# Performance work log

Measured on AMD Instinct MI355X. Metric: run time of the kernel, lower is better.

## Reference

```python
import jax, jax.numpy as jnp
import numpy as np

K = 2          # hops
N_HEAD = 34    # relation types
H = 100        # hidden size
BS = 32
N_NODE = 200
EPS = 1e-20
INIT_RANGE = 0.01


def setup_inputs() -> dict:
    key = jax.random.key(0)
    ks = jax.random.split(key, 7)
    X = jax.random.normal(ks[0], (BS, N_NODE, H), dtype=jnp.float32)
    A = (jax.random.uniform(ks[1], (BS, N_HEAD, N_NODE, N_NODE)) < 0.05).astype(jnp.float32)
    start_attn = jax.random.uniform(ks[2], (BS, N_NODE), dtype=jnp.float32)
    end_attn = jax.random.uniform(ks[3], (BS, N_NODE), dtype=jnp.float32)
    uni_attn = jax.random.uniform(ks[4], (BS, N_HEAD), dtype=jnp.float32)
    trans_attn = jax.random.uniform(ks[5], (BS, N_HEAD, N_HEAD), dtype=jnp.float32)
    # dense branch: diag_decompose=False, n_basis=0 -> (k, n_head+1, h, h)
    w_vs = jax.random.uniform(ks[6], (K, N_HEAD + 1, H, H), dtype=jnp.float32,
                              minval=-INIT_RANGE, maxval=INIT_RANGE)
    return dict(X=X, A=A, start_attn=start_attn, end_attn=end_attn,
                uni_attn=uni_attn, trans_attn=trans_attn, w_vs=w_vs)


def reference(X, A, start_attn, end_attn, uni_attn, trans_attn, w_vs):
    # _get_weights (n_basis == 0, diag_decompose == False)
    W = w_vs[:, :-1]   # (k, n_head, h, h)
    Wi = w_vs[:, -1]   # (k, h, h)
    W_pad = [jnp.eye(H, dtype=X.dtype)]
    for t in range(K - 1):
        W_pad = [Wi[K - 1 - t] @ W_pad[0]] + W_pad   # length k

    # ---- Z propagation ----
    Z0 = X * start_attn[:, :, None]                  # (b, n, h)
    Z_all = []
    Zprev = None                                     # (b, f, n, h) after a hop
    for t in range(K):
        if t == 0:
            Zin = jnp.broadcast_to(Z0[:, :, :, None], (BS, N_NODE, H, N_HEAD))
        else:
            # permute + bmm with trans_attn: mix over incoming head f -> g
            Zin = jnp.einsum('bfni,bfg->bnig', Zprev, trans_attn)
        # per-head feature transform: (b,n,i,f) x (f,i,o) -> (b,f,n,o)
        Zh = jnp.einsum('bnif,fio->bfno', Zin, W[t])
        Zh = Zh * uni_attn[:, :, None, None]
        # adjacency propagation per head: A (b,f,m,n) x Z (b,f,n,o)
        Zh = jnp.einsum('bfmn,bfno->bfmo', A, Zh)    # (b, f, n, h)
        # sum heads, project with W_pad[t], gate by end_attn
        Zt = jnp.einsum('bfno,oi->bni', Zh, W_pad[t])
        Zt = Zt * end_attn[:, :, None]
        Z_all.append(Zt)
        Zprev = Zh

    # ---- degree normalizer D ----
    D_all = []
    Dprev = None                                     # (b, f, n)
    for t in range(K):
        if t == 0:
            Din = jnp.broadcast_to(start_attn[:, None, :], (BS, N_HEAD, N_NODE))
        else:
            Din = jnp.einsum('bfn,bfg->bgn', Dprev, trans_attn)
        Dh = Din * uni_attn[:, :, None]
        Dh = jnp.einsum('bfmn,bfn->bfm', A, Dh)      # (b, f, n)
        D_all.append(Dh.sum(axis=1) * end_attn)
        Dprev = Dh

    # per-hop outputs, normalized; stacked as (k, b, n, h)
    out = jnp.stack([Z / (D[:, :, None] + EPS) for Z, D in zip(Z_all, D_all)])
    return out
```

## Files before the change

kernel.cpp:

```cpp
#include <hip/hip_runtime.h>
#include <hip/hip_bf16.h>

#define NHEAD 34
#define HDIM  100
#define NNODE 200
#define NBATCH 32
#define EPSV 1e-20f

typedef __attribute__((ext_vector_type(8))) short bf16x8;
typedef __attribute__((ext_vector_type(4))) float f32x4;
typedef __attribute__((ext_vector_type(16))) float f32x16;
typedef __attribute__((ext_vector_type(4))) unsigned int ux4;

__device__ inline unsigned short bf16rne(float x) {
    return __bfloat16_as_ushort(__float2bfloat16(x));
}
__device__ inline float bf16tof(unsigned short h) {
    unsigned u = ((unsigned)h) << 16;
    return __builtin_bit_cast(float, u);
}

__device__ inline void split3_8(const float* v, bf16x8& p0, bf16x8& p1, bf16x8& p2) {
    #pragma unroll
    for (int j = 0; j < 8; j++) {
        float x = v[j];
        unsigned short h0 = bf16rne(x); float r1 = x - bf16tof(h0);
        unsigned short h1 = bf16rne(r1); float r2 = r1 - bf16tof(h1);
        unsigned short h2 = bf16rne(r2);
        p0[j] = (short)h0; p1[j] = (short)h1; p2[j] = (short)h2;
    }
}

__device__ inline void split2s(float x, unsigned short& h0, unsigned short& h1) {
    h0 = bf16rne(x);
    h1 = bf16rne(x - bf16tof(h0));
}
__device__ inline void split2_pack8(const float* v, bf16x8& a0, bf16x8& a1) {
    #pragma unroll
    for (int j = 0; j < 8; j++) {
        unsigned short h0, h1; split2s(v[j], h0, h1);
        a0[j] = (short)h0; a1[j] = (short)h1;
    }
}

__device__ inline bf16x8 afrag_bits(unsigned byte) {
    ux4 p;
    #pragma unroll
    for (int r = 0; r < 4; r++) {
        p[r] = ((byte >> (2 * r)) & 1u) * 0x3F80u + ((byte >> (2 * r + 1)) & 1u) * 0x3F800000u;
    }
    return __builtin_bit_cast(bf16x8, p);
}

__global__ __launch_bounds__(1024) void a_bitmask(const float* __restrict__ A,
                                                  unsigned long long* __restrict__ bm) {
    int row = blockIdx.x * 16 + (threadIdx.x >> 6);
    int lane = threadIdx.x & 63;
    if (row >= NBATCH * NHEAD * NNODE) return;
    const float* Ar = A + (size_t)row * NNODE;
    unsigned long long w0 = __ballot(Ar[lane] != 0.0f);
    unsigned long long w1 = __ballot(Ar[64 + lane] != 0.0f);
    unsigned long long w2 = __ballot(Ar[128 + lane] != 0.0f);
    unsigned long long w3 = __ballot(lane < 8 ? (Ar[192 + lane] != 0.0f) : false);
    if (lane == 0) {
        unsigned long long* p = bm + (size_t)row * 4;
        p[0] = w0; p[1] = w1; p[2] = w2; p[3] = w3;
    }
}

__global__ __launch_bounds__(256) void wsplit(const float* __restrict__ wv,
                                              short* __restrict__ wfr) {
    int fw = blockIdx.x;
    const float* W = wv + (size_t)(fw / 34) * 350000 + (size_t)(fw % 34) * 10000;
    for (int s0 = threadIdx.x; s0 < 28 * 64; s0 += 256) {
        int frag = s0 >> 6;
        int l = s0 & 63;
        int nt = frag >> 2, ks = frag & 3;
        int n = nt * 16 + (l & 15);
        int kb = ks * 32 + ((l >> 4) << 3);
        float v[8];
        #pragma unroll
        for (int j = 0; j < 8; j++) {
            int k = kb + j;
            v[j] = (k < 100 && n < 100) ? W[k * 100 + n] : 0.0f;
        }
        bf16x8 p0, p1, p2;
        split3_8(v, p0, p1, p2);
        size_t base = (((size_t)fw * 28 + frag) * 3) * 512 + l * 8;
        *(bf16x8*)&wfr[base]        = p0;
        *(bf16x8*)&wfr[base + 512]  = p1;
        *(bf16x8*)&wfr[base + 1024] = p2;
    }
}

__global__ __launch_bounds__(256) void asplit(const float* __restrict__ X,
                                              const float* __restrict__ start,
                                              short* __restrict__ xfr) {
    int b = blockIdx.x;
    const float* Xb = X + (size_t)b * 20000;
    const float* st = start + (size_t)b * NNODE;
    for (int s0 = threadIdx.x; s0 < 52 * 64; s0 += 256) {
        int frag = s0 >> 6;
        int l = s0 & 63;
        int mt = frag >> 2, ks = frag & 3;
        int row = mt * 16 + (l & 15);
        int kb = ks * 32 + ((l >> 4) << 3);
        float sc = (row < 200) ? st[row] : 0.0f;
        float v[8];
        #pragma unroll
        for (int j = 0; j < 8; j++) {
            int k = kb + j;
            v[j] = (row < 200 && k < 100) ? Xb[row * 100 + k] * sc : 0.0f;
        }
        bf16x8 p0, p1, p2;
        split3_8(v, p0, p1, p2);
        size_t base = (((size_t)b * 52 + frag) * 3) * 512 + l * 8;
        *(bf16x8*)&xfr[base]        = p0;
        *(bf16x8*)&xfr[base + 512]  = p1;
        *(bf16x8*)&xfr[base + 1024] = p2;
    }
}

template <int T>
__global__ __launch_bounds__(1024, 8) void fused_zha(
    const unsigned* __restrict__ bm32,
    const short* __restrict__ xfr,
    const float* __restrict__ Sfp,
    const short* __restrict__ wfr_t,
    const float* __restrict__ uni,
    const float* __restrict__ start,
    const float* __restrict__ dvec_g,
    float* __restrict__ Zout, float* __restrict__ Dh)
{
    int ch = blockIdx.x & 1, f = blockIdx.x >> 1, b = blockIdx.y;
    size_t bf = (size_t)b * NHEAD + f;
    int tid = threadIdx.x;
    int l = tid & 63, w = tid >> 6;

    __shared__ __align__(16) short zpl[2][64][216];
    __shared__ unsigned mkl[8][225];

    const unsigned* bmw = bm32 + bf * 1600;
    for (int idx = tid; idx < 1600; idx += 1024) mkl[idx & 7][idx >> 3] = bmw[idx];
    if (tid < 200) mkl[tid / 25][200 + tid % 25] = 0u;

    float u = uni[b * NHEAD + f];

    if (ch == 1) {
        if (tid < 200) {
            float dv;
            if constexpr (T == 0) dv = start[b * NNODE + tid] * u;
            else                  dv = dvec_g[bf * NNODE + tid];
            unsigned short h0, h1; split2s(dv, h0, h1);
            zpl[0][36][tid] = (short)h0; zpl[1][36][tid] = (short)h1;
        } else if (tid < 232) {
            int r = 200 + ((tid - 200) & 15), s = (tid - 200) >> 4;
            zpl[s][36][r] = 0;
        }
    }

    const short* WF = wfr_t + (size_t)f * 28 * 3 * 512;
    int ntb = ch ? 4 : 0, nte = ch ? 7 : 4;
    int coff = ch * 64;
    for (int mt = w; mt < 13; mt += 16) {
        bf16x8 A0[4], A1[4];
        if constexpr (T == 0) {
            const short* AG = xfr + ((size_t)b * 52 + mt * 4) * 3 * 512;
            #pragma unroll
            for (int ks = 0; ks < 4; ks++) {
                A0[ks] = *(const bf16x8*)&AG[(ks * 3 + 0) * 512 + l * 8];
                A1[ks] = *(const bf16x8*)&AG[(ks * 3 + 1) * 512 + l * 8];
            }
        } else {
            const float* S = Sfp + bf * 20000;
            int row = mt * 16 + (l & 15);
            bool rok = row < 200;
            #pragma unroll
            for (int ks = 0; ks < 4; ks++) {
                int kb = ks * 32 + ((l >> 4) << 3);
                float4 z4 = make_float4(0.f, 0.f, 0.f, 0.f);
                float4 v0 = (rok && kb < 100)     ? *(const float4*)&S[row * 100 + kb]     : z4;
                float4 v1 = (rok && kb + 4 < 100) ? *(const float4*)&S[row * 100 + kb + 4] : z4;
                float vv[8] = {v0.x, v0.y, v0.z, v0.w, v1.x, v1.y, v1.z, v1.w};
                split2_pack8(vv, A0[ks], A1[ks]);
            }
        }
        for (int nt = ntb; nt < nte; nt++) {
            f32x4 acc = {0.f, 0.f, 0.f, 0.f};
            #pragma unroll
            for (int ks = 0; ks < 4; ks++) {
                const short* wp = &WF[(size_t)((nt * 4 + ks) * 3) * 512 + l * 8];
                bf16x8 B0 = *(const bf16x8*)&wp[0];
                bf16x8 B1 = *(const bf16x8*)&wp[512];
                acc = __builtin_amdgcn_mfma_f32_16x16x32_bf16(A0[ks], B0, acc, 0, 0, 0);
                acc = __builtin_amdgcn_mfma_f32_16x16x32_bf16(A1[ks], B0, acc, 0, 0, 0);
                acc = __builtin_amdgcn_mfma_f32_16x16x32_bf16(A0[ks], B1, acc, 0, 0, 0);
            }
            int c = nt * 16 + (l & 15);
            if (c < 100) {
                int nb = mt * 16 + ((l >> 4) << 2);
                short4 q0, q1;
                #pragma unroll
                for (int r = 0; r < 4; r++) {
                    unsigned short h0, h1; split2s(acc[r] * u, h0, h1);
                    ((short*)&q0)[r] = (short)h0;
                    ((short*)&q1)[r] = (short)h1;
                }
                *(short4*)&zpl[0][c - coff][nb] = q0;
                *(short4*)&zpl[1][c - coff][nb] = q1;
            }
        }
    }
    __syncthreads();

    int cl = l & 31, kg = l >> 5;
    int mt2 = w >> 1, cg = w & 1;
    int myl = cg * 32 + cl;
    bool act = (w < 14);

    f32x16 acc2;
    #pragma unroll
    for (int i = 0; i < 16; i++) acc2[i] = 0.f;

    if (act) {
        for (int ks = 0; ks < 13; ks++) {
            bf16x8 z0 = *(const bf16x8*)&zpl[0][myl][ks * 16 + kg * 8];
            bf16x8 z1 = *(const bf16x8*)&zpl[1][myl][ks * 16 + kg * 8];
            unsigned word = mkl[ks >> 1][mt2 * 32 + cl];
            unsigned byte = (word >> (((ks & 1) << 4) | (kg << 3))) & 0xFFu;
            bf16x8 af = afrag_bits(byte);
            acc2 = __builtin_amdgcn_mfma_f32_32x32x16_bf16(af, z0, acc2, 0, 0, 0);
            acc2 = __builtin_amdgcn_mfma_f32_32x32x16_bf16(af, z1, acc2, 0, 0, 0);
        }
    }
    __syncthreads();

    float* zs = (float*)&zpl[0][0][0];
    if (act) {
        int myg = coff + myl;
        if (myg <= 100) {
            #pragma unroll
            for (int r = 0; r < 16; r++) {
                int m = mt2 * 32 + (r & 3) + ((r >> 2) << 3) + (kg << 2);
                if (m < 200) zs[m * 68 + myl] = acc2[r];
            }
        }
    }
    __syncthreads();

    float* Zob = Zout + bf * 20000;
    if (ch == 0) {
        for (int idx = tid; idx < 3200; idx += 1024) {
            int m = idx >> 4, c4 = idx & 15;
            *(float4*)&Zob[m * 100 + c4 * 4] = *(const float4*)&zs[m * 68 + c4 * 4];
        }
    } else {
        float* Dhb = Dh + bf * NNODE;
        for (int idx = tid; idx < 2000; idx += 1024) {
            int m = idx / 10, c4 = idx % 10;
            if (c4 < 9) *(float4*)&Zob[m * 100 + 64 + c4 * 4] = *(const float4*)&zs[m * 68 + c4 * 4];
            else Dhb[m] = zs[m * 68 + 36];
        }
    }
}

__global__ __launch_bounds__(256) void out0_gemm(
    const float* __restrict__ src, const float* __restrict__ W,
    const float* __restrict__ rowscale, float* __restrict__ dst)
{
    int c = blockIdx.x, b = blockIdx.y;
    const float* S = src + (size_t)b * 20000;
    float* Dst = dst + (size_t)b * 20000;

    __shared__ __align__(16) float wl[10000];
    __shared__ __align__(16) float xl[5000];

    int tid = threadIdx.x;
    for (int idx = tid; idx < 10000; idx += 256) wl[idx] = W[idx];
    int base = c * 5000;
    for (int idx = tid; idx < 5000; idx += 256) xl[idx] = S[base + idx];
    __syncthreads();

    int q = tid % 25;
    int ty = tid / 25;
    if (ty < 10) {
        float4 acc[5];
        #pragma unroll
        for (int r = 0; r < 5; r++) acc[r] = make_float4(0.f, 0.f, 0.f, 0.f);
        #pragma unroll 2
        for (int i = 0; i < 100; i++) {
            float4 w4 = *(const float4*)&wl[i * 100 + q * 4];
            #pragma unroll
            for (int r = 0; r < 5; r++) {
                float x = xl[(ty + 10 * r) * 100 + i];
                acc[r].x += x * w4.x; acc[r].y += x * w4.y;
                acc[r].z += x * w4.z; acc[r].w += x * w4.w;
            }
        }
        #pragma unroll
        for (int r = 0; r < 5; r++) {
            int n = c * 50 + ty + 10 * r;
            float sc = rowscale[b * NNODE + n];
            float4 o4 = make_float4(acc[r].x * sc, acc[r].y * sc, acc[r].z * sc, acc[r].w * sc);
            *(float4*)&Dst[n * 100 + q * 4] = o4;
        }
    }
}

__global__ void dmix_rs(const float* __restrict__ Dh0, const float* __restrict__ trans,
                        const float* __restrict__ uni, const float* __restrict__ endat,
                        float* __restrict__ dvec1, float* __restrict__ rs0) {
    int b = blockIdx.x;
    __shared__ float tl[NHEAD * NHEAD];
    for (int idx = threadIdx.x; idx < NHEAD * NHEAD; idx += 256) tl[idx] = trans[b * NHEAD * NHEAD + idx];
    __syncthreads();
    int n = threadIdx.x;
    if (n < NNODE) {
        float dh[NHEAD];
        float s = 0.f;
        #pragma unroll
        for (int f = 0; f < NHEAD; f++) { dh[f] = Dh0[((size_t)b * NHEAD + f) * NNODE + n]; s += dh[f]; }
        float e = endat[b * NNODE + n];
        rs0[b * NNODE + n] = e / (e * s + EPSV);
        #pragma unroll
        for (int g = 0; g < NHEAD; g++) {
            float acc = 0.f;
            #pragma unroll
            for (int f = 0; f < NHEAD; f++) acc += dh[f] * tl[f * NHEAD + g];
            dvec1[((size_t)b * NHEAD + g) * NNODE + n] = uni[b * NHEAD + g] * acc;
        }
    }
}

__global__ void dsum_rs(const float* __restrict__ Dh, const float* __restrict__ endat,
                        float* __restrict__ rs) {
    int idx = blockIdx.x * 256 + threadIdx.x;
    if (idx >= NBATCH * NNODE) return;
    int b = idx / NNODE, m = idx % NNODE;
    float s = 0.f;
    #pragma unroll
    for (int f = 0; f < NHEAD; f++) s += Dh[((size_t)b * NHEAD + f) * NNODE + m];
    float e = endat[idx];
    rs[idx] = e / (e * s + EPSV);
}

__global__ __launch_bounds__(256) void hmix(
    const float* __restrict__ Zsrc, const float* __restrict__ trans,
    float* __restrict__ Zdst, float* __restrict__ Zsum)
{
    int b = blockIdx.y;
    int c2 = blockIdx.x * 256 + threadIdx.x;
    __shared__ __align__(8) float tl[NHEAD * NHEAD];
    for (int idx = threadIdx.x; idx < NHEAD * NHEAD; idx += 256) tl[idx] = trans[b * NHEAD * NHEAD + idx];
    __syncthreads();
    if (c2 >= 10000) return;
    const float2* Zb = (const float2*)(Zsrc + (size_t)b * NHEAD * 20000) + c2;
    float2 acc[NHEAD];
    #pragma unroll
    for (int g = 0; g < NHEAD; g++) acc[g] = make_float2(0.f, 0.f);
    float2 s = make_float2(0.f, 0.f);
    for (int f = 0; f < NHEAD; f++) {
        float2 vf = Zb[(size_t)f * 10000];
        s.x += vf.x; s.y += vf.y;
        const float2* row = (const float2*)&tl[f * NHEAD];
        #pragma unroll
        for (int gq = 0; gq < 17; gq++) {
            float2 t2 = row[gq];
            acc[2 * gq].x     += vf.x * t2.x; acc[2 * gq].y     += vf.y * t2.x;
            acc[2 * gq + 1].x += vf.x * t2.y; acc[2 * gq + 1].y += vf.y * t2.y;
        }
    }
    ((float2*)(Zsum + (size_t)b * 20000))[c2] = s;
    float2* Zd = (float2*)(Zdst + (size_t)b * NHEAD * 20000) + c2;
    #pragma unroll
    for (int g = 0; g < NHEAD; g++) Zd[(size_t)g * 10000] = acc[g];
}

__global__ void fsum_out(const float* __restrict__ Zacc, const float* __restrict__ rs,
                         float* __restrict__ out) {
    int idx = blockIdx.x * 256 + threadIdx.x;
    if (idx >= NBATCH * 10000) return;
    int b = idx / 10000;
    int c2 = idx % 10000;
    const float2* Zb = (const float2*)(Zacc + (size_t)b * NHEAD * 20000) + c2;
    float2 s = make_float2(0.f, 0.f);
    #pragma unroll
    for (int g = 0; g < NHEAD; g++) {
        float2 v = Zb[(size_t)g * 10000];
        s.x += v.x; s.y += v.y;
    }
    int n = (c2 * 2) / 100;
    float r = rs[b * NNODE + n];
    s.x *= r; s.y *= r;
    ((float2*)out)[idx] = s;
}

extern "C" void kernel_launch(void* const* d_in, const int* in_sizes, int n_in,
                              void* d_out, int out_size, void* d_ws, size_t ws_size,
                              hipStream_t stream) {
    (void)in_sizes; (void)n_in;
    const float* X     = (const float*)d_in[0];
    const float* A     = (const float*)d_in[1];
    const float* start = (const float*)d_in[2];
    const float* endat = (const float*)d_in[3];
    const float* uni   = (const float*)d_in[4];
    const float* trans = (const float*)d_in[5];
    const float* wv    = (const float*)d_in[6];
    float* out = (float*)d_out;
    float* ws  = (float*)d_ws;

    size_t off = 0;
    unsigned long long* bm = (unsigned long long*)(ws); off += 1740800;
    float* buf1  = ws + off; off += 21760000;
    float* buf2  = ws + off; off += 21760000;
    float* Dh0   = ws + off; off += 217600;
    float* dvec1 = ws + off; off += 217600;
    float* Dh1   = ws + off; off += 217600;
    float* rs0   = ws + off; off += 6400;
    float* rs1   = ws + off; off += 6400;
    float* Zsum0 = ws + off; off += 640000;
    short* wfr   = (short*)(ws + off); off += 1462272;
    short* xfr   = (short*)(ws + off); off += 1277952;
    if (ws_size < off * sizeof(float)) {
        hipMemsetAsync(d_out, 0x7F, (size_t)out_size * sizeof(float), stream);
        return;
    }

    const float* Wi1 = wv + 690000;
    const short* wfr0 = wfr;
    const short* wfr1 = wfr + (size_t)34 * 28 * 3 * 512;
    const unsigned* bm32 = (const unsigned*)bm;

    dim3 gBF(NHEAD * 2, NBATCH);

    a_bitmask<<<(NBATCH * NHEAD * NNODE + 15) / 16, 1024, 0, stream>>>(A, bm);
    wsplit<<<68, 256, 0, stream>>>(wv, wfr);
    asplit<<<32, 256, 0, stream>>>(X, start, xfr);

    fused_zha<0><<<gBF, 1024, 0, stream>>>(bm32, xfr, nullptr, wfr0, uni, start, nullptr, buf2, Dh0);
    dmix_rs<<<NBATCH, 256, 0, stream>>>(Dh0, trans, uni, endat, dvec1, rs0);
    hmix<<<dim3(40, NBATCH), 256, 0, stream>>>(buf2, trans, buf1, Zsum0);
    out0_gemm<<<dim3(4, NBATCH), 256, 0, stream>>>(Zsum0, Wi1, rs0, out);

    fused_zha<1><<<gBF, 1024, 0, stream>>>(bm32, nullptr, buf1, wfr1, uni, nullptr, dvec1, buf2, Dh1);
    dsum_rs<<<(NBATCH * NNODE + 255) / 256, 256, 0, stream>>>(Dh1, endat, rs1);
    fsum_out<<<(NBATCH * 10000 + 255) / 256, 256, 0, stream>>>(buf2, rs1, out + 640000);
}
```

Baseline: 335.1 us.

## Split fused_zha column work into four 32-column chunks with 512-thread blocks

The fused per-head kernel now splits the 100 output columns plus the degree column into four chunks of 32 instead of two of 64. Blocks shrink from 1024 to 512 threads, and the grid doubles to 136x32. Block indices are also remapped with an XCD-style swizzle so blocks of the same batch group together. The goal is better occupancy and load balance with smaller shared memory per block, at the cost of loading the adjacency bitmask once per chunk and recomputing the first-stage A fragments in more blocks.

```diff
diff --git a/kernel.cpp b/kernel.cpp
--- a/kernel.cpp
+++ b/kernel.cpp
@@ -122,7 +122,7 @@
 }
 
 template <int T>
-__global__ __launch_bounds__(1024, 8) void fused_zha(
+__global__ __launch_bounds__(512, 8) void fused_zha(
     const unsigned* __restrict__ bm32,
     const short* __restrict__ xfr,
     const float* __restrict__ Sfp,
@@ -132,37 +132,46 @@
     const float* __restrict__ dvec_g,
     float* __restrict__ Zout, float* __restrict__ Dh)
 {
-    int ch = blockIdx.x & 1, f = blockIdx.x >> 1, b = blockIdx.y;
+    int g = blockIdx.y * 136 + blockIdx.x;
+    int wk = (g & 7) * 544 + (g >> 3);
+    int b = wk / 136;
+    int rem = wk - b * 136;
+    int f = rem >> 2, ch = rem & 3;
     size_t bf = (size_t)b * NHEAD + f;
     int tid = threadIdx.x;
     int l = tid & 63, w = tid >> 6;
 
-    __shared__ __align__(16) short zpl[2][64][216];
+    __shared__ __align__(16) short zpl[2][32][216];
     __shared__ unsigned mkl[8][225];
 
     const unsigned* bmw = bm32 + bf * 1600;
-    for (int idx = tid; idx < 1600; idx += 1024) mkl[idx & 7][idx >> 3] = bmw[idx];
+    for (int idx = tid; idx < 1600; idx += 512) mkl[idx & 7][idx >> 3] = bmw[idx];
     if (tid < 200) mkl[tid / 25][200 + tid % 25] = 0u;
 
     float u = uni[b * NHEAD + f];
 
-    if (ch == 1) {
+    if (ch == 3) {
+        for (int idx = tid; idx < 27 * 216; idx += 512) {
+            int c = 5 + idx / 216, n = idx % 216;
+            zpl[0][c][n] = 0; zpl[1][c][n] = 0;
+        }
         if (tid < 200) {
             float dv;
             if constexpr (T == 0) dv = start[b * NNODE + tid] * u;
             else                  dv = dvec_g[bf * NNODE + tid];
             unsigned short h0, h1; split2s(dv, h0, h1);
-            zpl[0][36][tid] = (short)h0; zpl[1][36][tid] = (short)h1;
+            zpl[0][4][tid] = (short)h0; zpl[1][4][tid] = (short)h1;
         } else if (tid < 232) {
             int r = 200 + ((tid - 200) & 15), s = (tid - 200) >> 4;
-            zpl[s][36][r] = 0;
+            zpl[s][4][r] = 0;
         }
     }
 
     const short* WF = wfr_t + (size_t)f * 28 * 3 * 512;
-    int ntb = ch ? 4 : 0, nte = ch ? 7 : 4;
-    int coff = ch * 64;
-    for (int mt = w; mt < 13; mt += 16) {
+    int ntE = (ch < 3) ? 2 : 1;
+    int nt0 = (ch < 3) ? 2 * ch : 6;
+    int coff = ch * 32;
+    for (int mt = w; mt < 13; mt += 8) {
         bf16x8 A0[4], A1[4];
         if constexpr (T == 0) {
             const short* AG = xfr + ((size_t)b * 52 + mt * 4) * 3 * 512;
@@ -185,7 +194,8 @@
                 split2_pack8(vv, A0[ks], A1[ks]);
             }
         }
-        for (int nt = ntb; nt < nte; nt++) {
+        for (int ntl = 0; ntl < ntE; ntl++) {
+            int nt = nt0 + ntl;
             f32x4 acc = {0.f, 0.f, 0.f, 0.f};
             #pragma unroll
             for (int ks = 0; ks < 4; ks++) {
@@ -214,19 +224,15 @@
     __syncthreads();
 
     int cl = l & 31, kg = l >> 5;
-    int mt2 = w >> 1, cg = w & 1;
-    int myl = cg * 32 + cl;
-    bool act = (w < 14);
-
     f32x16 acc2;
     #pragma unroll
     for (int i = 0; i < 16; i++) acc2[i] = 0.f;
 
-    if (act) {
+    if (w < 7) {
         for (int ks = 0; ks < 13; ks++) {
-            bf16x8 z0 = *(const bf16x8*)&zpl[0][myl][ks * 16 + kg * 8];
-            bf16x8 z1 = *(const bf16x8*)&zpl[1][myl][ks * 16 + kg * 8];
-            unsigned word = mkl[ks >> 1][mt2 * 32 + cl];
+            bf16x8 z0 = *(const bf16x8*)&zpl[0][cl][ks * 16 + kg * 8];
+            bf16x8 z1 = *(const bf16x8*)&zpl[1][cl][ks * 16 + kg * 8];
+            unsigned word = mkl[ks >> 1][w * 32 + cl];
             unsigned byte = (word >> (((ks & 1) << 4) | (kg << 3))) & 0xFFu;
             bf16x8 af = afrag_bits(byte);
             acc2 = __builtin_amdgcn_mfma_f32_32x32x16_bf16(af, z0, acc2, 0, 0, 0);
@@ -236,30 +242,27 @@
     __syncthreads();
 
     float* zs = (float*)&zpl[0][0][0];
-    if (act) {
-        int myg = coff + myl;
-        if (myg <= 100) {
-            #pragma unroll
-            for (int r = 0; r < 16; r++) {
-                int m = mt2 * 32 + (r & 3) + ((r >> 2) << 3) + (kg << 2);
-                if (m < 200) zs[m * 68 + myl] = acc2[r];
-            }
+    if (w < 7) {
+        #pragma unroll
+        for (int r = 0; r < 16; r++) {
+            int m = w * 32 + (r & 3) + ((r >> 2) << 3) + (kg << 2);
+            if (m < 200) zs[m * 32 + cl] = acc2[r];
         }
     }
     __syncthreads();
 
     float* Zob = Zout + bf * 20000;
-    if (ch == 0) {
-        for (int idx = tid; idx < 3200; idx += 1024) {
-            int m = idx >> 4, c4 = idx & 15;
-            *(float4*)&Zob[m * 100 + c4 * 4] = *(const float4*)&zs[m * 68 + c4 * 4];
+    if (ch < 3) {
+        for (int idx = tid; idx < 1600; idx += 512) {
+            int m = idx >> 3, c4 = idx & 7;
+            *(float4*)&Zob[m * 100 + coff + c4 * 4] = *(const float4*)&zs[m * 32 + c4 * 4];
         }
     } else {
         float* Dhb = Dh + bf * NNODE;
-        for (int idx = tid; idx < 2000; idx += 1024) {
-            int m = idx / 10, c4 = idx % 10;
-            if (c4 < 9) *(float4*)&Zob[m * 100 + 64 + c4 * 4] = *(const float4*)&zs[m * 68 + c4 * 4];
-            else Dhb[m] = zs[m * 68 + 36];
+        for (int idx = tid; idx < 400; idx += 512) {
+            int m = idx >> 1;
+            if (idx & 1) Dhb[m] = zs[m * 32 + 4];
+            else *(float4*)&Zob[m * 100 + 96] = *(const float4*)&zs[m * 32];
         }
     }
 }
@@ -431,18 +434,18 @@
     const short* wfr1 = wfr + (size_t)34 * 28 * 3 * 512;
     const unsigned* bm32 = (const unsigned*)bm;
 
-    dim3 gBF(NHEAD * 2, NBATCH);
+    dim3 gBF(NHEAD * 4, NBATCH);
 
     a_bitmask<<<(NBATCH * NHEAD * NNODE + 15) / 16, 1024, 0, stream>>>(A, bm);
     wsplit<<<68, 256, 0, stream>>>(wv, wfr);
     asplit<<<32, 256, 0, stream>>>(X, start, xfr);
 
-    fused_zha<0><<<gBF, 1024, 0, stream>>>(bm32, xfr, nullptr, wfr0, uni, start, nullptr, buf2, Dh0);
+    fused_zha<0><<<gBF, 512, 0, stream>>>(bm32, xfr, nullptr, wfr0, uni, start, nullptr, buf2, Dh0);
     dmix_rs<<<NBATCH, 256, 0, stream>>>(Dh0, trans, uni, endat, dvec1, rs0);
     hmix<<<dim3(40, NBATCH), 256, 0, stream>>>(buf2, trans, buf1, Zsum0);
     out0_gemm<<<dim3(4, NBATCH), 256, 0, stream>>>(Zsum0, Wi1, rs0, out);
 
-    fused_zha<1><<<gBF, 1024, 0, stream>>>(bm32, nullptr, buf1, wfr1, uni, nullptr, dvec1, buf2, Dh1);
+    fused_zha<1><<<gBF, 512, 0, stream>>>(bm32, nullptr, buf1, wfr1, uni, nullptr, dvec1, buf2, Dh1);
     dsum_rs<<<(NBATCH * NNODE + 255) / 256, 256, 0, stream>>>(Dh1, endat, rs1);
     fsum_out<<<(NBATCH * 10000 + 255) / 256, 256, 0, stream>>>(buf2, rs1, out + 640000);
 }
```

Result: slower. 366.2 us (+9.3%).
